# Kernel optimization log

Measured on AMD Instinct MI355X. Metric: run time of the kernel, lower is better.

## Reference

```python
import jax
jax.config.update("jax_enable_x64", True)
import jax.numpy as jnp
import numpy as np

INPUT_DIM = 2048
NUM_BINS = 32
RMS_EPS = 1e-4  # RunningMeanStd initial count


def setup_inputs() -> dict:
    key = jax.random.key(0)
    k1, k2 = jax.random.split(key)
    features = jax.random.normal(k1, (64, 256, INPUT_DIM), dtype=jnp.float32)
    # register_buffer: randn(input_dim, num_bins) / sqrt(input_dim)
    random_projection = jax.random.normal(k2, (INPUT_DIM, NUM_BINS), dtype=jnp.float32) / np.sqrt(INPUT_DIM)
    return {"features": features, "random_projection": random_projection}


def _occurrence_counts(keys):
    """For each element, 1 + number of earlier elements with the same key.
    Stable argsort keeps original order inside each duplicate run, so the
    rank within a run equals the sequential visit count."""
    n = keys.shape[0]
    order = jnp.argsort(keys)  # stable
    sk = keys[order]
    idx = jnp.arange(n, dtype=jnp.int64)
    new_run = jnp.concatenate([jnp.ones((1,), bool), sk[1:] != sk[:-1]])
    starts = jax.lax.cummax(jnp.where(new_run, idx, 0))
    counts_sorted = idx - starts + 1
    return jnp.zeros(n, jnp.int64).at[order].set(counts_sorted)


def reference(features, random_projection):
    batch, seq, feat = features.shape
    x = features.reshape(-1, feat)
    n = x.shape[0]

    # RunningMeanStd.update from fresh state (mean=0, var=1, count=1e-4)
    bm = jnp.mean(x, axis=0)
    bv = jnp.var(x, axis=0, ddof=1)  # torch .var(dim=0) is unbiased
    tot = RMS_EPS + n
    mean = bm * (n / tot)  # delta = bm - 0
    m2 = 1.0 * RMS_EPS + bv * n + (bm ** 2) * (RMS_EPS * n / tot)
    var = m2 / tot
    sigma = jnp.sqrt(var + 1e-8)

    normalized = (x - mean) / sigma
    projected = normalized @ random_projection  # [n, num_bins]
    bits = (projected > 0).astype(jnp.int64)
    powers = (2 ** jnp.arange(min(NUM_BINS, 63), dtype=jnp.int64))
    h = (bits[:, : powers.shape[0]] * powers).sum(axis=-1)  # < 2^32

    env = jnp.arange(n, dtype=jnp.int64) % batch  # default env_indices path
    keys = h * batch + env  # unique per (env, hash), fits int64
    counts = _occurrence_counts(keys)

    rewards = 1.0 / jnp.sqrt(counts.astype(features.dtype))
    return rewards.reshape(batch, seq, 1)
```

## Files before the change

### kernel.cpp

```cpp
#include <hip/hip_runtime.h>
#include <math.h>

#define FEAT 2048
#define NBINS 32
#define NROWS 16384
#define NCLS 64

typedef __attribute__((ext_vector_type(8))) short short8;
typedef __attribute__((ext_vector_type(4))) float f32x4;

static __device__ __forceinline__ unsigned short f2bf(float f) {
    unsigned u = __float_as_uint(f);
    unsigned r = (u + 0x7FFFu + ((u >> 16) & 1u)) >> 16;
    return (unsigned short)r;
}

__global__ __launch_bounds__(256) void k1_stats(const float* __restrict__ x,
                                                float* __restrict__ pS1,
                                                float* __restrict__ pS2,
                                                int rpb) {
    const int b = blockIdx.x, t = threadIdx.x;
    const float4* xb = reinterpret_cast<const float4*>(x) + (size_t)b * rpb * (FEAT / 4);
    float4 s1a = make_float4(0.f, 0.f, 0.f, 0.f);
    float4 s1b = make_float4(0.f, 0.f, 0.f, 0.f);
    float4 s2a = make_float4(0.f, 0.f, 0.f, 0.f);
    float4 s2b = make_float4(0.f, 0.f, 0.f, 0.f);
    for (int r = 0; r < rpb; ++r) {
        const float4 va = xb[(size_t)r * (FEAT / 4) + t];
        const float4 vb = xb[(size_t)r * (FEAT / 4) + t + 256];
        s1a.x += va.x; s1a.y += va.y; s1a.z += va.z; s1a.w += va.w;
        s2a.x += va.x * va.x; s2a.y += va.y * va.y; s2a.z += va.z * va.z; s2a.w += va.w * va.w;
        s1b.x += vb.x; s1b.y += vb.y; s1b.z += vb.z; s1b.w += vb.w;
        s2b.x += vb.x * vb.x; s2b.y += vb.y * vb.y; s2b.z += vb.z * vb.z; s2b.w += vb.w * vb.w;
    }
    float4* o1 = reinterpret_cast<float4*>(pS1 + (size_t)b * FEAT);
    float4* o2 = reinterpret_cast<float4*>(pS2 + (size_t)b * FEAT);
    o1[t] = s1a; o1[t + 256] = s1b;
    o2[t] = s2a; o2[t + 256] = s2b;
}

__global__ __launch_bounds__(256) void k2_final(const float* __restrict__ pS1,
                                                const float* __restrict__ pS2,
                                                const float* __restrict__ P,
                                                float* __restrict__ ms,
                                                unsigned short* __restrict__ QT,
                                                int SB) {
    __shared__ double sh1[8][32];
    __shared__ double sh2[8][32];
    const int t = threadIdx.x;
    const int ci = t & 31, seg = t >> 5;
    const int c = blockIdx.x * 32 + ci;
    const int segN = SB >> 3;
    double S1 = 0.0, S2 = 0.0;
    for (int i = 0; i < segN; ++i) {
        const int k = seg * segN + i;
        S1 += (double)pS1[(size_t)k * FEAT + c];
        S2 += (double)pS2[(size_t)k * FEAT + c];
    }
    sh1[seg][ci] = S1; sh2[seg][ci] = S2;
    __syncthreads();
    if (t < 32) {
        double s1 = 0.0, s2 = 0.0;
        #pragma unroll
        for (int s = 0; s < 8; ++s) { s1 += sh1[s][t]; s2 += sh2[s][t]; }
        const int cc = blockIdx.x * 32 + t;
        const double n = (double)NROWS;
        const double bm = s1 / n;
        const double bv = (s2 - s1 * s1 / n) / (n - 1.0);
        const double tot = 1e-4 + n;
        const double mean = bm * (n / tot);
        const double m2 = 1e-4 + bv * n + bm * bm * (1e-4 * n / tot);
        const double var = m2 / tot;
        const double isig = 1.0 / sqrt(var + 1e-8);
        ms[cc] = (float)(mean * isig);
        for (int b = 0; b < NBINS; ++b) {
            QT[(size_t)b * FEAT + cc] = f2bf((float)((double)P[(size_t)cc * NBINS + b] * isig));
        }
    }
}

__global__ __launch_bounds__(256) void k2b_offset(const float* __restrict__ ms,
                                                  const float* __restrict__ P,
                                                  float* __restrict__ offs) {
    __shared__ double sh[256];
    const int b = blockIdx.x, t = threadIdx.x;
    double s = 0.0;
    for (int f = t; f < FEAT; f += 256) s += (double)ms[f] * (double)P[(size_t)f * NBINS + b];
    sh[t] = s;
    __syncthreads();
    for (int st = 128; st > 0; st >>= 1) {
        if (t < st) sh[t] += sh[t + st];
        __syncthreads();
    }
    if (t == 0) offs[b] = (float)sh[0];
}

__global__ __launch_bounds__(256) void k3_mfma(const float* __restrict__ x,
                                               const unsigned short* __restrict__ QT,
                                               const float* __restrict__ offs,
                                               unsigned int* __restrict__ hout) {
    __shared__ unsigned short xbf[64 * 128];
    __shared__ unsigned short qbf[32 * 128];
    const int t = threadIdx.x;
    const int w = t >> 6, l = t & 63;
    const int lrow = l & 15, lk = l >> 4;
    const int bid = blockIdx.x;
    const int r0 = bid * 64;

    f32x4 acc0 = {0.f, 0.f, 0.f, 0.f};
    f32x4 acc1 = {0.f, 0.f, 0.f, 0.f};

    float4 xr[2][8];
    int4 qr[2][2];

    #pragma unroll
    for (int j = 0; j < 8; ++j) {
        const int q = t + 256 * j;
        const int row = q >> 5, c4 = q & 31;
        xr[0][j] = *reinterpret_cast<const float4*>(x + (size_t)(r0 + row) * FEAT + c4 * 4);
    }
    #pragma unroll
    for (int j = 0; j < 2; ++j) {
        const int G = t + 256 * j;
        const int bin = G >> 4, g = G & 15;
        const int gsrc = g ^ (bin & 7);
        qr[0][j] = *reinterpret_cast<const int4*>(QT + (size_t)bin * FEAT + gsrc * 8);
    }

    #pragma unroll
    for (int ch = 0; ch < 16; ++ch) {
        const int cur = ch & 1, nxt = cur ^ 1;
        __syncthreads();
        if (ch < 15) {
            #pragma unroll
            for (int j = 0; j < 8; ++j) {
                const int q = t + 256 * j;
                const int row = q >> 5, c4 = q & 31;
                xr[nxt][j] = *reinterpret_cast<const float4*>(
                    x + (size_t)(r0 + row) * FEAT + (ch + 1) * 128 + c4 * 4);
            }
            #pragma unroll
            for (int j = 0; j < 2; ++j) {
                const int G = t + 256 * j;
                const int bin = G >> 4, g = G & 15;
                const int gsrc = g ^ (bin & 7);
                qr[nxt][j] = *reinterpret_cast<const int4*>(
                    QT + (size_t)bin * FEAT + (ch + 1) * 128 + gsrc * 8);
            }
        }
        #pragma unroll
        for (int j = 0; j < 8; ++j) {
            const int q = t + 256 * j;
            const int row = q >> 5, c4 = q & 31;
            const int g = c4 >> 1, half = c4 & 1;
            const int gs = g ^ (row & 7);
            const float4 v = xr[cur][j];
            int2 pk;
            pk.x = (int)f2bf(v.x) | ((int)f2bf(v.y) << 16);
            pk.y = (int)f2bf(v.z) | ((int)f2bf(v.w) << 16);
            *reinterpret_cast<int2*>(&xbf[row * 128 + gs * 8 + half * 4]) = pk;
        }
        #pragma unroll
        for (int j = 0; j < 2; ++j) {
            const int G = t + 256 * j;
            const int bin = G >> 4, g = G & 15;
            *reinterpret_cast<int4*>(&qbf[bin * 128 + g * 8]) = qr[cur][j];
        }
        __syncthreads();
        #pragma unroll
        for (int ks = 0; ks < 4; ++ks) {
            const int gsw = (ks * 4 + lk) ^ (lrow & 7);
            const short8 a = *reinterpret_cast<const short8*>(
                &xbf[(w * 16 + lrow) * 128 + gsw * 8]);
            const short8 b0 = *reinterpret_cast<const short8*>(
                &qbf[lrow * 128 + gsw * 8]);
            const short8 b1 = *reinterpret_cast<const short8*>(
                &qbf[(16 + lrow) * 128 + gsw * 8]);
            acc0 = __builtin_amdgcn_mfma_f32_16x16x32_bf16(a, b0, acc0, 0, 0, 0);
            acc1 = __builtin_amdgcn_mfma_f32_16x16x32_bf16(a, b1, acc1, 0, 0, 0);
        }
    }

    const float o0 = offs[lrow];
    const float o1 = offs[16 + lrow];
    #pragma unroll
    for (int r = 0; r < 4; ++r) {
        const unsigned long long m0 = __ballot(acc0[r] > o0);
        const unsigned long long m1 = __ballot(acc1[r] > o1);
        if (lrow == 0) {
            const unsigned int h =
                (unsigned int)((m0 >> (16 * lk)) & 0xFFFFull) |
                ((unsigned int)((m1 >> (16 * lk)) & 0xFFFFull) << 16);
            const int irow = w * 16 + lk * 4 + r;
            hout[(size_t)irow * 256 + bid] = h;
        }
    }
}

__global__ __launch_bounds__(256) void k4_count(const unsigned int* __restrict__ hcls,
                                                float* __restrict__ out) {
    __shared__ unsigned int hh[256];
    const int c = blockIdx.x, t = threadIdx.x;
    hh[t] = hcls[(size_t)c * 256 + t];
    __syncthreads();
    const unsigned int mine = hh[t];
    int cnt = 1;
    for (int j = 0; j < 256; ++j) {
        cnt += (j < t && hh[j] == mine) ? 1 : 0;
    }
    out[(size_t)t * NCLS + c] = 1.0f / sqrtf((float)cnt);
}

extern "C" void kernel_launch(void* const* d_in, const int* in_sizes, int n_in,
                              void* d_out, int out_size, void* d_ws, size_t ws_size,
                              hipStream_t stream) {
    const float* x = (const float*)d_in[0];
    const float* P = (const float*)d_in[1];
    float* out = (float*)d_out;
    float* ws = (float*)d_ws;

    const int SB = (ws_size >= (size_t)4600000) ? 256 : 64;
    const int rpb = NROWS / SB;

    float* pS1 = ws;
    float* pS2 = pS1 + (size_t)SB * FEAT;
    float* ms = pS2 + (size_t)SB * FEAT;
    float* offsB = ms + FEAT;
    unsigned short* QT = (unsigned short*)(offsB + NBINS);
    unsigned int* h = (unsigned int*)(QT + (size_t)FEAT * NBINS);

    k1_stats<<<SB, 256, 0, stream>>>(x, pS1, pS2, rpb);
    k2_final<<<64, 256, 0, stream>>>(pS1, pS2, P, ms, QT, SB);
    k2b_offset<<<32, 256, 0, stream>>>(ms, P, offsB);
    k3_mfma<<<256, 256, 0, stream>>>(x, QT, offsB, h);
    k4_count<<<NCLS, 256, 0, stream>>>(h, out);
}
```

Baseline: 80.68 us.

## Emit bf16 fragment-layout copy of features during stats pass; stream MFMA operands directly

The stats kernel now also converts each row of the input to bf16 and writes it into a workspace buffer laid out in MFMA fragment order. The projection matrix is likewise pre-packed into fragment order. The MFMA kernel then loads its operands straight from global memory, with no LDS staging, no conversion and no barriers. The intent is to halve the bytes the GEMM pass reads and to remove its shared-memory overhead. In exchange it adds a 64 MB write in the first pass and hard-codes SB=256, which assumes the workspace is at least about 72 MB.

```diff
diff --git a/kernel.cpp b/kernel.cpp
--- a/kernel.cpp
+++ b/kernel.cpp
@@ -5,33 +5,47 @@
 #define NBINS 32
 #define NROWS 16384
 #define NCLS 64
+#define SB 256
+#define RPB 64
 
 typedef __attribute__((ext_vector_type(8))) short short8;
 typedef __attribute__((ext_vector_type(4))) float f32x4;
 
-static __device__ __forceinline__ unsigned short f2bf(float f) {
-    unsigned u = __float_as_uint(f);
-    unsigned r = (u + 0x7FFFu + ((u >> 16) & 1u)) >> 16;
-    return (unsigned short)r;
+static __device__ __forceinline__ unsigned int pk2bf(float a, float b) {
+    unsigned ua = __float_as_uint(a);
+    unsigned ub = __float_as_uint(b);
+    ua = (ua + 0x7FFFu + ((ua >> 16) & 1u)) >> 16;
+    ub = (ub + 0x7FFFu + ((ub >> 16) & 1u)) & 0xFFFF0000u;
+    return ua | ub;
 }
 
 __global__ __launch_bounds__(256) void k1_stats(const float* __restrict__ x,
                                                 float* __restrict__ pS1,
                                                 float* __restrict__ pS2,
-                                                int rpb) {
+                                                unsigned int* __restrict__ xbf) {
     const int b = blockIdx.x, t = threadIdx.x;
-    const float4* xb = reinterpret_cast<const float4*>(x) + (size_t)b * rpb * (FEAT / 4);
-    float4 s1a = make_float4(0.f, 0.f, 0.f, 0.f);
-    float4 s1b = make_float4(0.f, 0.f, 0.f, 0.f);
-    float4 s2a = make_float4(0.f, 0.f, 0.f, 0.f);
-    float4 s2b = make_float4(0.f, 0.f, 0.f, 0.f);
-    for (int r = 0; r < rpb; ++r) {
+    const float4* xb = reinterpret_cast<const float4*>(x) + (size_t)b * RPB * (FEAT / 4);
+    const int k0a = 4 * t;
+    const int k0b = 4 * t + 1024;
+    const int cpA = ((k0a >> 7) * 4 + ((k0a >> 5) & 3)) * 1024 + (((k0a >> 3) & 3) << 8) + ((k0a & 7) << 1);
+    const int cpB = ((k0b >> 7) * 4 + ((k0b >> 5) & 3)) * 1024 + (((k0b >> 3) & 3) << 8) + ((k0b & 7) << 1);
+    char* tile = reinterpret_cast<char*>(xbf) + (size_t)b * 262144;
+
+    float4 s1a = make_float4(0.f,0.f,0.f,0.f), s1b = make_float4(0.f,0.f,0.f,0.f);
+    float4 s2a = make_float4(0.f,0.f,0.f,0.f), s2b = make_float4(0.f,0.f,0.f,0.f);
+    for (int r = 0; r < RPB; ++r) {
         const float4 va = xb[(size_t)r * (FEAT / 4) + t];
         const float4 vb = xb[(size_t)r * (FEAT / 4) + t + 256];
         s1a.x += va.x; s1a.y += va.y; s1a.z += va.z; s1a.w += va.w;
         s2a.x += va.x * va.x; s2a.y += va.y * va.y; s2a.z += va.z * va.z; s2a.w += va.w * va.w;
         s1b.x += vb.x; s1b.y += vb.y; s1b.z += vb.z; s1b.w += vb.w;
         s2b.x += vb.x * vb.x; s2b.y += vb.y * vb.y; s2b.z += vb.z * vb.z; s2b.w += vb.w * vb.w;
+        const int rp = (r >> 4) * 65536 + (r & 15) * 16;
+        uint2 pa, pb;
+        pa.x = pk2bf(va.x, va.y); pa.y = pk2bf(va.z, va.w);
+        pb.x = pk2bf(vb.x, vb.y); pb.y = pk2bf(vb.z, vb.w);
+        *reinterpret_cast<uint2*>(tile + cpA + rp) = pa;
+        *reinterpret_cast<uint2*>(tile + cpB + rp) = pb;
     }
     float4* o1 = reinterpret_cast<float4*>(pS1 + (size_t)b * FEAT);
     float4* o2 = reinterpret_cast<float4*>(pS2 + (size_t)b * FEAT);
@@ -43,17 +57,16 @@
                                                 const float* __restrict__ pS2,
                                                 const float* __restrict__ P,
                                                 float* __restrict__ ms,
-                                                unsigned short* __restrict__ QT,
-                                                int SB) {
+                                                unsigned int* __restrict__ QTf) {
     __shared__ double sh1[8][32];
     __shared__ double sh2[8][32];
+    __shared__ float isig_sh[32];
     const int t = threadIdx.x;
     const int ci = t & 31, seg = t >> 5;
     const int c = blockIdx.x * 32 + ci;
-    const int segN = SB >> 3;
     double S1 = 0.0, S2 = 0.0;
-    for (int i = 0; i < segN; ++i) {
-        const int k = seg * segN + i;
+    for (int i = 0; i < 32; ++i) {
+        const int k = seg * 32 + i;
         S1 += (double)pS1[(size_t)k * FEAT + c];
         S2 += (double)pS2[(size_t)k * FEAT + c];
     }
@@ -73,10 +86,25 @@
         const double var = m2 / tot;
         const double isig = 1.0 / sqrt(var + 1e-8);
         ms[cc] = (float)(mean * isig);
-        for (int b = 0; b < NBINS; ++b) {
-            QT[(size_t)b * FEAT + cc] = f2bf((float)((double)P[(size_t)cc * NBINS + b] * isig));
-        }
-    }
+        isig_sh[t] = (float)isig;
+    }
+    __syncthreads();
+    const int nb = t >> 7;
+    const int lane = (t & 127) >> 1;
+    const int half = t & 1;
+    const int lrow = lane & 15, lk = lane >> 4;
+    const int bin = nb * 16 + lrow;
+    const int ccl = lk * 8 + half * 4;
+    const int cc = blockIdx.x * 32 + ccl;
+    unsigned int w0 = pk2bf(P[(size_t)cc * NBINS + bin] * isig_sh[ccl],
+                            P[(size_t)(cc + 1) * NBINS + bin] * isig_sh[ccl + 1]);
+    unsigned int w1 = pk2bf(P[(size_t)(cc + 2) * NBINS + bin] * isig_sh[ccl + 2],
+                            P[(size_t)(cc + 3) * NBINS + bin] * isig_sh[ccl + 3]);
+    const int ch = blockIdx.x >> 2, ks = blockIdx.x & 3;
+    char* dst = reinterpret_cast<char*>(QTf) +
+                (size_t)(((nb * 16 + ch) * 4 + ks) * 1024 + lane * 16 + half * 8);
+    uint2 pk; pk.x = w0; pk.y = w1;
+    *reinterpret_cast<uint2*>(dst) = pk;
 }
 
 __global__ __launch_bounds__(256) void k2b_offset(const float* __restrict__ ms,
@@ -95,90 +123,29 @@
     if (t == 0) offs[b] = (float)sh[0];
 }
 
-__global__ __launch_bounds__(256) void k3_mfma(const float* __restrict__ x,
-                                               const unsigned short* __restrict__ QT,
+__global__ __launch_bounds__(256) void k3_mfma(const unsigned int* __restrict__ xbf,
+                                               const unsigned int* __restrict__ QTf,
                                                const float* __restrict__ offs,
                                                unsigned int* __restrict__ hout) {
-    __shared__ unsigned short xbf[64 * 128];
-    __shared__ unsigned short qbf[32 * 128];
     const int t = threadIdx.x;
     const int w = t >> 6, l = t & 63;
     const int lrow = l & 15, lk = l >> 4;
     const int bid = blockIdx.x;
-    const int r0 = bid * 64;
+
+    const short8* ap  = reinterpret_cast<const short8*>(xbf) + (size_t)bid * 16384 + w * 4096 + l;
+    const short8* b0p = reinterpret_cast<const short8*>(QTf) + l;
+    const short8* b1p = b0p + 4096;
 
     f32x4 acc0 = {0.f, 0.f, 0.f, 0.f};
     f32x4 acc1 = {0.f, 0.f, 0.f, 0.f};
 
-    float4 xr[2][8];
-    int4 qr[2][2];
-
-    #pragma unroll
-    for (int j = 0; j < 8; ++j) {
-        const int q = t + 256 * j;
-        const int row = q >> 5, c4 = q & 31;
-        xr[0][j] = *reinterpret_cast<const float4*>(x + (size_t)(r0 + row) * FEAT + c4 * 4);
-    }
-    #pragma unroll
-    for (int j = 0; j < 2; ++j) {
-        const int G = t + 256 * j;
-        const int bin = G >> 4, g = G & 15;
-        const int gsrc = g ^ (bin & 7);
-        qr[0][j] = *reinterpret_cast<const int4*>(QT + (size_t)bin * FEAT + gsrc * 8);
-    }
-
-    #pragma unroll
-    for (int ch = 0; ch < 16; ++ch) {
-        const int cur = ch & 1, nxt = cur ^ 1;
-        __syncthreads();
-        if (ch < 15) {
-            #pragma unroll
-            for (int j = 0; j < 8; ++j) {
-                const int q = t + 256 * j;
-                const int row = q >> 5, c4 = q & 31;
-                xr[nxt][j] = *reinterpret_cast<const float4*>(
-                    x + (size_t)(r0 + row) * FEAT + (ch + 1) * 128 + c4 * 4);
-            }
-            #pragma unroll
-            for (int j = 0; j < 2; ++j) {
-                const int G = t + 256 * j;
-                const int bin = G >> 4, g = G & 15;
-                const int gsrc = g ^ (bin & 7);
-                qr[nxt][j] = *reinterpret_cast<const int4*>(
-                    QT + (size_t)bin * FEAT + (ch + 1) * 128 + gsrc * 8);
-            }
-        }
-        #pragma unroll
-        for (int j = 0; j < 8; ++j) {
-            const int q = t + 256 * j;
-            const int row = q >> 5, c4 = q & 31;
-            const int g = c4 >> 1, half = c4 & 1;
-            const int gs = g ^ (row & 7);
-            const float4 v = xr[cur][j];
-            int2 pk;
-            pk.x = (int)f2bf(v.x) | ((int)f2bf(v.y) << 16);
-            pk.y = (int)f2bf(v.z) | ((int)f2bf(v.w) << 16);
-            *reinterpret_cast<int2*>(&xbf[row * 128 + gs * 8 + half * 4]) = pk;
-        }
-        #pragma unroll
-        for (int j = 0; j < 2; ++j) {
-            const int G = t + 256 * j;
-            const int bin = G >> 4, g = G & 15;
-            *reinterpret_cast<int4*>(&qbf[bin * 128 + g * 8]) = qr[cur][j];
-        }
-        __syncthreads();
-        #pragma unroll
-        for (int ks = 0; ks < 4; ++ks) {
-            const int gsw = (ks * 4 + lk) ^ (lrow & 7);
-            const short8 a = *reinterpret_cast<const short8*>(
-                &xbf[(w * 16 + lrow) * 128 + gsw * 8]);
-            const short8 b0 = *reinterpret_cast<const short8*>(
-                &qbf[lrow * 128 + gsw * 8]);
-            const short8 b1 = *reinterpret_cast<const short8*>(
-                &qbf[(16 + lrow) * 128 + gsw * 8]);
-            acc0 = __builtin_amdgcn_mfma_f32_16x16x32_bf16(a, b0, acc0, 0, 0, 0);
-            acc1 = __builtin_amdgcn_mfma_f32_16x16x32_bf16(a, b1, acc1, 0, 0, 0);
-        }
+    #pragma unroll 8
+    for (int ss = 0; ss < 64; ++ss) {
+        const short8 a  = ap[ss * 64];
+        const short8 b0 = b0p[ss * 64];
+        const short8 b1 = b1p[ss * 64];
+        acc0 = __builtin_amdgcn_mfma_f32_16x16x32_bf16(a, b0, acc0, 0, 0, 0);
+        acc1 = __builtin_amdgcn_mfma_f32_16x16x32_bf16(a, b1, acc1, 0, 0, 0);
     }
 
     const float o0 = offs[lrow];
@@ -217,21 +184,19 @@
     const float* x = (const float*)d_in[0];
     const float* P = (const float*)d_in[1];
     float* out = (float*)d_out;
-    float* ws = (float*)d_ws;
-
-    const int SB = (ws_size >= (size_t)4600000) ? 256 : 64;
-    const int rpb = NROWS / SB;
-
-    float* pS1 = ws;
-    float* pS2 = pS1 + (size_t)SB * FEAT;
-    float* ms = pS2 + (size_t)SB * FEAT;
+    char* ws = (char*)d_ws;
+
+    float* pS1 = (float*)(ws);
+    float* pS2 = (float*)(ws + (size_t)SB * FEAT * 4);
+    float* ms  = (float*)(ws + (size_t)2 * SB * FEAT * 4);
     float* offsB = ms + FEAT;
-    unsigned short* QT = (unsigned short*)(offsB + NBINS);
-    unsigned int* h = (unsigned int*)(QT + (size_t)FEAT * NBINS);
-
-    k1_stats<<<SB, 256, 0, stream>>>(x, pS1, pS2, rpb);
-    k2_final<<<64, 256, 0, stream>>>(pS1, pS2, P, ms, QT, SB);
+    unsigned int* xbf = (unsigned int*)(ws + (size_t)8 * 1024 * 1024);
+    unsigned int* QTf = (unsigned int*)(ws + (size_t)8 * 1024 * 1024 + (size_t)64 * 1024 * 1024);
+    unsigned int* h   = (unsigned int*)(ws + (size_t)8 * 1024 * 1024 + (size_t)64 * 1024 * 1024 + 131072);
+
+    k1_stats<<<SB, 256, 0, stream>>>(x, pS1, pS2, xbf);
+    k2_final<<<64, 256, 0, stream>>>(pS1, pS2, P, ms, QTf);
     k2b_offset<<<32, 256, 0, stream>>>(ms, P, offsB);
-    k3_mfma<<<256, 256, 0, stream>>>(x, QT, offsB, h);
+    k3_mfma<<<256, 256, 0, stream>>>(xbf, QTf, offsB, h);
     k4_count<<<NCLS, 256, 0, stream>>>(h, out);
 }
```

Result: faster. 70.34 us (-12.8%).
